# Optimization experiments

Hardware: AMD Instinct MI355X
Metric: run time of the kernel (lower is better)

The kernel has to match this reference:

```python
import jax, jax.numpy as jnp
import numpy as np
import math

HIDDEN = 256
HEADS = 8
HEAD_DIM = HIDDEN // HEADS
SCALE = math.sqrt(HEAD_DIM)


def setup_inputs() -> dict:
    key = jax.random.key(0)
    ks = jax.random.split(key, 10)
    B, N = 2, 4096
    x = jax.random.normal(ks[0], (B, N, HIDDEN), dtype=jnp.float32)
    pos = jax.random.normal(ks[1], (B, N, 3), dtype=jnp.float32)
    s = 1.0 / math.sqrt(HIDDEN)
    Wq = jax.random.normal(ks[2], (HIDDEN, HIDDEN), dtype=jnp.float32) * s
    bq = jnp.zeros((HIDDEN,), dtype=jnp.float32)
    Wk = jax.random.normal(ks[3], (HIDDEN, HIDDEN), dtype=jnp.float32) * s
    bk = jnp.zeros((HIDDEN,), dtype=jnp.float32)
    Wv = jax.random.normal(ks[4], (HIDDEN, HIDDEN), dtype=jnp.float32) * s
    bv = jnp.zeros((HIDDEN,), dtype=jnp.float32)
    Wo = jax.random.normal(ks[5], (HIDDEN, HIDDEN), dtype=jnp.float32) * s
    bo = jnp.zeros((HIDDEN,), dtype=jnp.float32)
    return {"x": x, "pos": pos, "Wq": Wq, "bq": bq, "Wk": Wk, "bk": bk,
            "Wv": Wv, "bv": bv, "Wo": Wo, "bo": bo}


def _pairwise_dist(pos):
    # Euclidean cdist via the norm trick; clip for numerical safety.
    sq = jnp.sum(pos * pos, axis=-1)  # [B, N]
    d2 = sq[:, :, None] + sq[:, None, :] - 2.0 * jnp.einsum('bic,bjc->bij', pos, pos)
    return jnp.sqrt(jnp.maximum(d2, 0.0))  # [B, N, N]


def reference(x, pos, Wq, bq, Wk, bk, Wv, bv, Wo, bo):
    B, N, _ = x.shape
    # projections -> [B, H, N, Dh]
    def split_heads(t):
        return t.reshape(B, N, HEADS, HEAD_DIM).transpose(0, 2, 1, 3)
    q = split_heads(x @ Wq.T + bq)
    k = split_heads(x @ Wk.T + bk)
    v = split_heads(x @ Wv.T + bv)
    scores = jnp.einsum('bhid,bhjd->bhij', q, k) / SCALE
    dist_bias = -_pairwise_dist(pos) / 10.0  # [B, N, N]
    scores = scores + dist_bias[:, None, :, :]
    attn = jax.nn.softmax(scores, axis=-1)
    out = jnp.einsum('bhij,bhjd->bhid', attn, v)
    out = out.transpose(0, 2, 1, 3).reshape(B, N, HIDDEN)
    return out @ Wo.T + bo
```

## Files before the change

### kernel.cpp

```cpp
#include <hip/hip_runtime.h>

#define BATCH 2
#define SEQ   4096
#define HID   256
#define NHEAD 8
#define DH    32
#define THR_L2 11.5f
#define QSCALE 0.25501639769925074f
#define BIASC (-0.14426950408889634f)

typedef __attribute__((ext_vector_type(8))) _Float16 half8;
typedef __attribute__((ext_vector_type(4))) _Float16 half4;
typedef __attribute__((ext_vector_type(2))) __fp16   fp16x2;
typedef __attribute__((ext_vector_type(4))) float    f32x4;
typedef __attribute__((ext_vector_type(4))) unsigned int uint4v;

__device__ __forceinline__ float fast_exp2(float x) {
    return __builtin_amdgcn_exp2f(x);
}

__global__ void cvt_f32_f16(const float* __restrict__ src,
                            _Float16* __restrict__ dst, int n) {
    int i = (blockIdx.x * blockDim.x + threadIdx.x) * 4;
    if (i >= n) return;
    f32x4 v = *reinterpret_cast<const f32x4*>(src + i);
    half4 h;
#pragma unroll
    for (int c = 0; c < 4; ++c) h[c] = (_Float16)v[c];
    *reinterpret_cast<half4*>(dst + i) = h;
}

__global__ void cvt_w4(const float* __restrict__ a, const float* __restrict__ b,
                       const float* __restrict__ c, const float* __restrict__ d,
                       _Float16* __restrict__ dst) {
    const float* srcs[4] = {a, b, c, d};
    const float* s = srcs[blockIdx.y];
    const int i = (blockIdx.x * blockDim.x + threadIdx.x) * 4;
    f32x4 v = *reinterpret_cast<const f32x4*>(s + i);
    half4 h;
#pragma unroll
    for (int k = 0; k < 4; ++k) h[k] = (_Float16)v[k];
    *reinterpret_cast<half4*>(dst + (size_t)blockIdx.y * HID * HID + i) = h;
}

__global__ __launch_bounds__(256) void qkv_proj(
    const _Float16* __restrict__ xh, const _Float16* __restrict__ Wh,
    const float* __restrict__ bq, const float* __restrict__ bk,
    const float* __restrict__ bv,
    _Float16* __restrict__ Qh, _Float16* __restrict__ Kh,
    _Float16* __restrict__ Vt)
{
    const int z   = blockIdx.z;
    const int m0  = blockIdx.x * 64;
    const int n0  = blockIdx.y * 64;
    const int tid = threadIdx.x;
    const int w   = tid >> 6, lane = tid & 63;
    const int lr  = lane & 15, lg = lane >> 4;
    const int wr  = (w >> 1) * 32, wc = (w & 1) * 32;

    const _Float16* Wp = Wh + (size_t)z * HID * HID;
    const float* bias = (z == 0) ? bq : (z == 1) ? bk : bv;

    f32x4 acc[2][2] = {};
    const int ar = m0 + wr + lr;
    const int br = n0 + wc + lr;
#pragma unroll
    for (int ks = 0; ks < 8; ++ks) {
        const int ko = ks * 32 + lg * 8;
        half8 a0 = *reinterpret_cast<const half8*>(xh + (size_t)ar * HID + ko);
        half8 a1 = *reinterpret_cast<const half8*>(xh + (size_t)(ar + 16) * HID + ko);
        half8 b0 = *reinterpret_cast<const half8*>(Wp + (size_t)br * HID + ko);
        half8 b1 = *reinterpret_cast<const half8*>(Wp + (size_t)(br + 16) * HID + ko);
        acc[0][0] = __builtin_amdgcn_mfma_f32_16x16x32_f16(a0, b0, acc[0][0], 0, 0, 0);
        acc[0][1] = __builtin_amdgcn_mfma_f32_16x16x32_f16(a0, b1, acc[0][1], 0, 0, 0);
        acc[1][0] = __builtin_amdgcn_mfma_f32_16x16x32_f16(a1, b0, acc[1][0], 0, 0, 0);
        acc[1][1] = __builtin_amdgcn_mfma_f32_16x16x32_f16(a1, b1, acc[1][1], 0, 0, 0);
    }
#pragma unroll
    for (int mf = 0; mf < 2; ++mf)
#pragma unroll
    for (int nf = 0; nf < 2; ++nf)
#pragma unroll
    for (int r = 0; r < 4; ++r) {
        const int m  = m0 + wr + mf * 16 + lg * 4 + r;
        const int o  = n0 + wc + nf * 16 + lr;
        const int bb = m >> 12, nn = m & (SEQ - 1);
        const int hh = o >> 5,  dd = o & (DH - 1);
        float v = acc[mf][nf][r] + bias[o];
        if (z == 0) {
            Qh[(((size_t)(bb * NHEAD + hh) * SEQ) + nn) * DH + dd] =
                (_Float16)(v * QSCALE);
        } else if (z == 1) {
            Kh[(((size_t)(bb * NHEAD + hh) * SEQ) + nn) * DH + dd] = (_Float16)v;
        } else {
            const int pp = (nn & ~31) | ((nn & 12) << 1) | ((nn & 16) >> 2) | (nn & 3);
            Vt[(((size_t)(bb * NHEAD + hh) * DH) + dd) * SEQ + pp] = (_Float16)v;
        }
    }
}

__device__ __forceinline__ void attn_tile(
    int s, half8 (&kc)[4], half8 (&kn)[4],
    unsigned long long& ka, unsigned long long& va0, unsigned long long& va1,
    half8 aq, const float* __restrict__ biasRow, float* xw,
    float& mrun, float& lsum, f32x4& acc0, f32x4& acc1, int lane, int lg)
{
    half8 vc0, vc1, vc2, vc3;
    asm volatile(
        "global_load_dwordx4 %0, %[va0], off\n\t"
        "global_load_dwordx4 %1, %[va1], off\n\t"
        "global_load_dwordx4 %2, %[va0], off offset:64\n\t"
        "global_load_dwordx4 %3, %[va1], off offset:64\n\t"
        "global_load_dwordx4 %4, %[ka], off\n\t"
        "global_load_dwordx4 %5, %[ka], off offset:1024\n\t"
        "global_load_dwordx4 %6, %[ka], off offset:2048\n\t"
        "global_load_dwordx4 %7, %[ka], off offset:3072"
        : "=&v"(vc0), "=&v"(vc1), "=&v"(vc2), "=&v"(vc3),
          "=&v"(kn[0]), "=&v"(kn[1]), "=&v"(kn[2]), "=&v"(kn[3])
        : [va0]"v"(va0), [va1]"v"(va1), [ka]"v"(ka));
    va0 += 128; va1 += 128; ka += 4096;

    asm volatile("s_waitcnt vmcnt(8)");
    __builtin_amdgcn_sched_barrier(0);
    f32x4 vv[4];
    __builtin_amdgcn_s_setprio(1);
#pragma unroll
    for (int cf = 0; cf < 4; ++cf) {
        f32x4 cb = *reinterpret_cast<const f32x4*>(
            biasRow + s * 64 + cf * 16 + lg * 4);
        vv[cf] = __builtin_amdgcn_mfma_f32_16x16x32_f16(kc[cf], aq, cb, 0, 0, 0);
    }
    __builtin_amdgcn_s_setprio(0);

    float m0 = fmaxf(fmaxf(vv[0][0], vv[0][1]), vv[0][2]);
    float m1 = fmaxf(fmaxf(vv[0][3], vv[1][0]), vv[1][1]);
    float m2 = fmaxf(fmaxf(vv[1][2], vv[1][3]), vv[2][0]);
    float m3 = fmaxf(fmaxf(vv[2][1], vv[2][2]), vv[2][3]);
    float m4 = fmaxf(fmaxf(vv[3][0], vv[3][1]), vv[3][2]);
    float tmax = fmaxf(fmaxf(fmaxf(m0, m1), fmaxf(m2, m3)),
                       fmaxf(m4, vv[3][3]));

    if (!__all(tmax <= mrun + THR_L2)) {
        float tm = tmax;
        tm = fmaxf(tm, __shfl_xor(tm, 16, 64));
        tm = fmaxf(tm, __shfl_xor(tm, 32, 64));
        const float mnew  = fmaxf(mrun, tm);
        const float alpha = fast_exp2(mrun - mnew);
        if (lane < 16) xw[lane] = alpha;
        f32x4 a4 = *reinterpret_cast<const f32x4*>(&xw[lg * 4]);
        lsum *= alpha;
        mrun = mnew;
        acc0 *= a4;
        acc1 *= a4;
    }

    float e00 = fast_exp2(vv[0][0] - mrun), e01 = fast_exp2(vv[0][1] - mrun);
    float e02 = fast_exp2(vv[0][2] - mrun), e03 = fast_exp2(vv[0][3] - mrun);
    float e10 = fast_exp2(vv[1][0] - mrun), e11 = fast_exp2(vv[1][1] - mrun);
    float e12 = fast_exp2(vv[1][2] - mrun), e13 = fast_exp2(vv[1][3] - mrun);
    float e20 = fast_exp2(vv[2][0] - mrun), e21 = fast_exp2(vv[2][1] - mrun);
    float e22 = fast_exp2(vv[2][2] - mrun), e23 = fast_exp2(vv[2][3] - mrun);
    float e30 = fast_exp2(vv[3][0] - mrun), e31 = fast_exp2(vv[3][1] - mrun);
    float e32 = fast_exp2(vv[3][2] - mrun), e33 = fast_exp2(vv[3][3] - mrun);
    lsum += ((e00 + e01) + (e02 + e03)) + ((e10 + e11) + (e12 + e13)) +
            ((e20 + e21) + (e22 + e23)) + ((e30 + e31) + (e32 + e33));

    uint4v u0, u1;
    u0[0] = __builtin_bit_cast(unsigned int, __builtin_amdgcn_cvt_pkrtz(e00, e01));
    u0[1] = __builtin_bit_cast(unsigned int, __builtin_amdgcn_cvt_pkrtz(e02, e03));
    u0[2] = __builtin_bit_cast(unsigned int, __builtin_amdgcn_cvt_pkrtz(e10, e11));
    u0[3] = __builtin_bit_cast(unsigned int, __builtin_amdgcn_cvt_pkrtz(e12, e13));
    u1[0] = __builtin_bit_cast(unsigned int, __builtin_amdgcn_cvt_pkrtz(e20, e21));
    u1[1] = __builtin_bit_cast(unsigned int, __builtin_amdgcn_cvt_pkrtz(e22, e23));
    u1[2] = __builtin_bit_cast(unsigned int, __builtin_amdgcn_cvt_pkrtz(e30, e31));
    u1[3] = __builtin_bit_cast(unsigned int, __builtin_amdgcn_cvt_pkrtz(e32, e33));
    half8 pa0 = __builtin_bit_cast(half8, u0);
    half8 pa1 = __builtin_bit_cast(half8, u1);

    asm volatile("s_waitcnt vmcnt(4)");
    __builtin_amdgcn_sched_barrier(0);
    __builtin_amdgcn_s_setprio(1);
    acc0 = __builtin_amdgcn_mfma_f32_16x16x32_f16(pa0, vc0, acc0, 0, 0, 0);
    acc1 = __builtin_amdgcn_mfma_f32_16x16x32_f16(pa0, vc1, acc1, 0, 0, 0);
    acc0 = __builtin_amdgcn_mfma_f32_16x16x32_f16(pa1, vc2, acc0, 0, 0, 0);
    acc1 = __builtin_amdgcn_mfma_f32_16x16x32_f16(pa1, vc3, acc1, 0, 0, 0);
    __builtin_amdgcn_s_setprio(0);
}

__global__ __launch_bounds__(512, 4) void attn_kernel(
    const _Float16* __restrict__ Qh, const _Float16* __restrict__ Kh,
    const _Float16* __restrict__ Vt, const float* __restrict__ pos,
    _Float16* __restrict__ AO)
{
    __shared__ __align__(16) float pi4[16][4];
    __shared__ __align__(16) float pj4[512][4];
    __shared__ __align__(16) float biasL[16][516];
    __shared__ __align__(16) float xposeL[NHEAD][16];

    const int g    = blockIdx.x;
    const int x    = g & 7;
    const int b    = x >> 2;
    const int i0   = ((g >> 3) * 4 + (x & 3)) * 16;
    const int tid  = threadIdx.x;
    const int w    = tid >> 6;
    const int lane = tid & 63;
    const int lr   = lane & 15, lg = lane >> 4;

    if (tid < 16) {
        const float* p = pos + (size_t)(b * SEQ + i0 + tid) * 3;
        float xx = p[0], yy = p[1], zz = p[2];
        pi4[tid][0] = xx; pi4[tid][1] = yy; pi4[tid][2] = zz;
        pi4[tid][3] = xx * xx + yy * yy + zz * zz;
    }

    const size_t bhh = (size_t)(b * NHEAD + w);
    const half8 aq = *reinterpret_cast<const half8*>(
        Qh + (bhh * SEQ + i0 + lr) * DH + lg * 8);

    unsigned long long ka  = (unsigned long long)(Kh + bhh * SEQ * DH +
                                                  (size_t)lr * DH + lg * 8);
    unsigned long long va0 = (unsigned long long)(Vt + bhh * DH * SEQ +
                                                  (size_t)lr * SEQ + lg * 8);
    unsigned long long va1 = va0 + (size_t)16 * SEQ * 2;

    f32x4 acc0 = {}, acc1 = {};
    float mrun = -1e30f, lsum = 0.f;

    float* xw = &xposeL[w][0];
    const float* biasRow = &biasL[lr][0];

    half8 kA[4], kB[4];
    asm volatile(
        "global_load_dwordx4 %0, %[ka], off\n\t"
        "global_load_dwordx4 %1, %[ka], off offset:1024\n\t"
        "global_load_dwordx4 %2, %[ka], off offset:2048\n\t"
        "global_load_dwordx4 %3, %[ka], off offset:3072"
        : "=&v"(kA[0]), "=&v"(kA[1]), "=&v"(kA[2]), "=&v"(kA[3])
        : [ka]"v"(ka));
    ka += 4096;

    for (int ch = 0; ch < SEQ / 512; ++ch) {
        __syncthreads();
        {
            const float* p = pos + (size_t)(b * SEQ + ch * 512 + tid) * 3;
            float xx = p[0], yy = p[1], zz = p[2];
            pj4[tid][0] = xx; pj4[tid][1] = yy; pj4[tid][2] = zz;
            pj4[tid][3] = xx * xx + yy * yy + zz * zz;
        }
        __syncthreads();
        {
            const int br  = tid & 15;
            const int c0  = (tid >> 4) * 16;
            const float xi = pi4[br][0], yi = pi4[br][1], zi = pi4[br][2], si = pi4[br][3];
#pragma unroll
            for (int k4 = 0; k4 < 4; ++k4) {
                f32x4 o;
#pragma unroll
                for (int k = 0; k < 4; ++k) {
                    const float* pj = &pj4[c0 + k4 * 4 + k][0];
                    float dot = xi * pj[0] + yi * pj[1] + zi * pj[2];
                    float d2  = si + pj[3] - 2.f * dot;
                    o[k] = BIASC * sqrtf(fmaxf(d2, 0.f));
                }
                *reinterpret_cast<f32x4*>(&biasL[br][c0 + k4 * 4]) = o;
            }
        }
        __syncthreads();

        for (int s = 0; s < 4; ++s) {
            attn_tile(2 * s,     kA, kB, ka, va0, va1, aq, biasRow, xw,
                      mrun, lsum, acc0, acc1, lane, lg);
            attn_tile(2 * s + 1, kB, kA, ka, va0, va1, aq, biasRow, xw,
                      mrun, lsum, acc0, acc1, lane, lg);
        }
    }
    asm volatile("s_waitcnt vmcnt(0)");

    lsum += __shfl_xor(lsum, 16, 64);
    lsum += __shfl_xor(lsum, 32, 64);
    const float inv = 1.f / lsum;
    if (lane < 16) xw[lane] = inv;
    f32x4 i4 = *reinterpret_cast<const f32x4*>(&xw[lg * 4]);
#pragma unroll
    for (int t = 0; t < 4; ++t) {
        const size_t row = (size_t)(b * SEQ + i0 + lg * 4 + t) * HID + w * DH;
        AO[row + lr]      = (_Float16)(acc0[t] * i4[t]);
        AO[row + 16 + lr] = (_Float16)(acc1[t] * i4[t]);
    }
}

__global__ __launch_bounds__(256) void out_proj(
    const _Float16* __restrict__ AO, const _Float16* __restrict__ Woh,
    const float* __restrict__ bo, float* __restrict__ out)
{
    const int m0  = blockIdx.x * 64;
    const int n0  = blockIdx.y * 64;
    const int tid = threadIdx.x;
    const int w   = tid >> 6, lane = tid & 63;
    const int lr  = lane & 15, lg = lane >> 4;
    const int wr  = (w >> 1) * 32, wc = (w & 1) * 32;

    f32x4 acc[2][2] = {};
    const int ar = m0 + wr + lr;
    const int br = n0 + wc + lr;
#pragma unroll
    for (int ks = 0; ks < 8; ++ks) {
        const int ko = ks * 32 + lg * 8;
        half8 a0 = *reinterpret_cast<const half8*>(AO + (size_t)ar * HID + ko);
        half8 a1 = *reinterpret_cast<const half8*>(AO + (size_t)(ar + 16) * HID + ko);
        half8 b0 = *reinterpret_cast<const half8*>(Woh + (size_t)br * HID + ko);
        half8 b1 = *reinterpret_cast<const half8*>(Woh + (size_t)(br + 16) * HID + ko);
        acc[0][0] = __builtin_amdgcn_mfma_f32_16x16x32_f16(a0, b0, acc[0][0], 0, 0, 0);
        acc[0][1] = __builtin_amdgcn_mfma_f32_16x16x32_f16(a0, b1, acc[0][1], 0, 0, 0);
        acc[1][0] = __builtin_amdgcn_mfma_f32_16x16x32_f16(a1, b0, acc[1][0], 0, 0, 0);
        acc[1][1] = __builtin_amdgcn_mfma_f32_16x16x32_f16(a1, b1, acc[1][1], 0, 0, 0);
    }
#pragma unroll
    for (int mf = 0; mf < 2; ++mf)
#pragma unroll
    for (int nf = 0; nf < 2; ++nf)
#pragma unroll
    for (int r = 0; r < 4; ++r) {
        const int m = m0 + wr + mf * 16 + lg * 4 + r;
        const int o = n0 + wc + nf * 16 + lr;
        out[(size_t)m * HID + o] = acc[mf][nf][r] + bo[o];
    }
}

extern "C" void kernel_launch(void* const* d_in, const int* in_sizes, int n_in,
                              void* d_out, int out_size, void* d_ws, size_t ws_size,
                              hipStream_t stream)
{
    const float* x   = (const float*)d_in[0];
    const float* pos = (const float*)d_in[1];
    const float* Wq  = (const float*)d_in[2];
    const float* bq  = (const float*)d_in[3];
    const float* Wk  = (const float*)d_in[4];
    const float* bk  = (const float*)d_in[5];
    const float* Wv  = (const float*)d_in[6];
    const float* bv  = (const float*)d_in[7];
    const float* Wo  = (const float*)d_in[8];
    const float* bo  = (const float*)d_in[9];
    float* out = (float*)d_out;

    char* ws = (char*)d_ws;
    _Float16* Qh = (_Float16*)(ws);
    _Float16* Kh = (_Float16*)(ws + (4  << 20));
    _Float16* Vt = (_Float16*)(ws + (8  << 20));
    _Float16* xh = (_Float16*)(ws + (12 << 20));
    _Float16* AO = xh;
    _Float16* Wh = (_Float16*)(ws + (16 << 20));

    const int NX = BATCH * SEQ * HID;
    const int NW = HID * HID;
    cvt_f32_f16<<<NX / 1024, 256, 0, stream>>>(x, xh, NX);
    cvt_w4<<<dim3(NW / 1024, 4), 256, 0, stream>>>(Wq, Wk, Wv, Wo, Wh);

    qkv_proj<<<dim3(BATCH * SEQ / 64, HID / 64, 3), 256, 0, stream>>>(
        xh, Wh, bq, bk, bv, Qh, Kh, Vt);

    attn_kernel<<<512, 512, 0, stream>>>(Qh, Kh, Vt, pos, AO);

    out_proj<<<dim3(BATCH * SEQ / 64, HID / 64), 256, 0, stream>>>(
        AO, Wh + 3 * NW, bo, out);
}
```

Measured before the change: 236.4 us.

## Split attention key range across two wave groups and merge softmax partials

```diff
diff --git a/kernel.cpp b/kernel.cpp
--- a/kernel.cpp
+++ b/kernel.cpp
@@ -187,15 +187,14 @@
     __builtin_amdgcn_s_setprio(0);
 }
 
-__global__ __launch_bounds__(512, 4) void attn_kernel(
+__global__ __launch_bounds__(1024, 4) void attn_kernel(
     const _Float16* __restrict__ Qh, const _Float16* __restrict__ Kh,
     const _Float16* __restrict__ Vt, const float* __restrict__ pos,
     _Float16* __restrict__ AO)
 {
+    __shared__ __align__(16) float smem[10368];
     __shared__ __align__(16) float pi4[16][4];
-    __shared__ __align__(16) float pj4[512][4];
-    __shared__ __align__(16) float biasL[16][516];
-    __shared__ __align__(16) float xposeL[NHEAD][16];
+    __shared__ __align__(16) float xposeL[16][16];
 
     const int g    = blockIdx.x;
     const int x    = g & 7;
@@ -203,8 +202,14 @@
     const int i0   = ((g >> 3) * 4 + (x & 3)) * 16;
     const int tid  = threadIdx.x;
     const int w    = tid >> 6;
+    const int hh   = w & 7;
+    const int jh   = w >> 3;
     const int lane = tid & 63;
     const int lr   = lane & 15, lg = lane >> 4;
+    const int jbase = jh * (SEQ / 2);
+
+    float* pj4   = smem;
+    float* biasL = smem + 2048;
 
     if (tid < 16) {
         const float* p = pos + (size_t)(b * SEQ + i0 + tid) * 3;
@@ -213,21 +218,21 @@
         pi4[tid][3] = xx * xx + yy * yy + zz * zz;
     }
 
-    const size_t bhh = (size_t)(b * NHEAD + w);
+    const size_t bhh = (size_t)(b * NHEAD + hh);
     const half8 aq = *reinterpret_cast<const half8*>(
         Qh + (bhh * SEQ + i0 + lr) * DH + lg * 8);
 
     unsigned long long ka  = (unsigned long long)(Kh + bhh * SEQ * DH +
-                                                  (size_t)lr * DH + lg * 8);
+                                 (size_t)(jbase + lr) * DH + lg * 8);
     unsigned long long va0 = (unsigned long long)(Vt + bhh * DH * SEQ +
-                                                  (size_t)lr * SEQ + lg * 8);
+                                 (size_t)lr * SEQ + jbase + lg * 8);
     unsigned long long va1 = va0 + (size_t)16 * SEQ * 2;
 
     f32x4 acc0 = {}, acc1 = {};
     float mrun = -1e30f, lsum = 0.f;
 
     float* xw = &xposeL[w][0];
-    const float* biasRow = &biasL[lr][0];
+    const float* biasRow = biasL + jh * 4160 + lr * 260;
 
     half8 kA[4], kB[4];
     asm volatile(
@@ -239,35 +244,38 @@
         : [ka]"v"(ka));
     ka += 4096;
 
-    for (int ch = 0; ch < SEQ / 512; ++ch) {
+    for (int ch = 0; ch < (SEQ / 2) / 256; ++ch) {
+        __syncthreads();
+        if (tid < 512) {
+            const int hf = tid >> 8, jc = tid & 255;
+            const float* p = pos +
+                (size_t)(b * SEQ + hf * (SEQ / 2) + ch * 256 + jc) * 3;
+            float xx = p[0], yy = p[1], zz = p[2];
+            float* q = pj4 + (hf * 256 + jc) * 4;
+            q[0] = xx; q[1] = yy; q[2] = zz; q[3] = xx * xx + yy * yy + zz * zz;
+        }
         __syncthreads();
         {
-            const float* p = pos + (size_t)(b * SEQ + ch * 512 + tid) * 3;
-            float xx = p[0], yy = p[1], zz = p[2];
-            pj4[tid][0] = xx; pj4[tid][1] = yy; pj4[tid][2] = zz;
-            pj4[tid][3] = xx * xx + yy * yy + zz * zz;
-        }
-        __syncthreads();
-        {
-            const int br  = tid & 15;
-            const int c0  = (tid >> 4) * 16;
+            const int br = tid & 15;
+            const int hf = (tid >> 4) & 1;
+            const int c0 = (tid >> 5) * 8;
             const float xi = pi4[br][0], yi = pi4[br][1], zi = pi4[br][2], si = pi4[br][3];
 #pragma unroll
-            for (int k4 = 0; k4 < 4; ++k4) {
+            for (int k4 = 0; k4 < 2; ++k4) {
                 f32x4 o;
 #pragma unroll
                 for (int k = 0; k < 4; ++k) {
-                    const float* pj = &pj4[c0 + k4 * 4 + k][0];
+                    const float* pj = pj4 + (hf * 256 + c0 + k4 * 4 + k) * 4;
                     float dot = xi * pj[0] + yi * pj[1] + zi * pj[2];
                     float d2  = si + pj[3] - 2.f * dot;
                     o[k] = BIASC * sqrtf(fmaxf(d2, 0.f));
                 }
-                *reinterpret_cast<f32x4*>(&biasL[br][c0 + k4 * 4]) = o;
+                *reinterpret_cast<f32x4*>(&biasL[hf * 4160 + br * 260 + c0 + k4 * 4]) = o;
             }
         }
         __syncthreads();
 
-        for (int s = 0; s < 4; ++s) {
+        for (int s = 0; s < 2; ++s) {
             attn_tile(2 * s,     kA, kB, ka, va0, va1, aq, biasRow, xw,
                       mrun, lsum, acc0, acc1, lane, lg);
             attn_tile(2 * s + 1, kB, kA, ka, va0, va1, aq, biasRow, xw,
@@ -278,14 +286,38 @@
 
     lsum += __shfl_xor(lsum, 16, 64);
     lsum += __shfl_xor(lsum, 32, 64);
-    const float inv = 1.f / lsum;
-    if (lane < 16) xw[lane] = inv;
-    f32x4 i4 = *reinterpret_cast<const f32x4*>(&xw[lg * 4]);
+
+    __syncthreads();
+    float* accL = smem;
+    float* mlL  = smem + 8192;
+    float* accW = accL + w * 512;
 #pragma unroll
     for (int t = 0; t < 4; ++t) {
-        const size_t row = (size_t)(b * SEQ + i0 + lg * 4 + t) * HID + w * DH;
-        AO[row + lr]      = (_Float16)(acc0[t] * i4[t]);
-        AO[row + 16 + lr] = (_Float16)(acc1[t] * i4[t]);
+        accW[(lg * 4 + t) * 32 + lr]      = acc0[t];
+        accW[(lg * 4 + t) * 32 + 16 + lr] = acc1[t];
+    }
+    if (lane < 16) {
+        mlL[(w * 16 + lane) * 2 + 0] = mrun;
+        mlL[(w * 16 + lane) * 2 + 1] = lsum;
+    }
+    __syncthreads();
+    if (w < 8) {
+#pragma unroll
+        for (int t = 0; t < 4; ++t) {
+            const int row = lg * 4 + t;
+            const float m0 = mlL[(w * 16 + row) * 2],       l0 = mlL[(w * 16 + row) * 2 + 1];
+            const float m1 = mlL[((w + 8) * 16 + row) * 2], l1 = mlL[((w + 8) * 16 + row) * 2 + 1];
+            const float mm = fmaxf(m0, m1);
+            const float e0 = fast_exp2(m0 - mm), e1 = fast_exp2(m1 - mm);
+            const float inv = 1.f / (l0 * e0 + l1 * e1);
+            const size_t rowoff = (size_t)(b * SEQ + i0 + row) * HID + w * DH;
+            AO[rowoff + lr] = (_Float16)(
+                (accL[w * 512 + row * 32 + lr] * e0 +
+                 accL[(w + 8) * 512 + row * 32 + lr] * e1) * inv);
+            AO[rowoff + 16 + lr] = (_Float16)(
+                (accL[w * 512 + row * 32 + 16 + lr] * e0 +
+                 accL[(w + 8) * 512 + row * 32 + 16 + lr] * e1) * inv);
+        }
     }
 }
 
@@ -359,7 +391,7 @@
     qkv_proj<<<dim3(BATCH * SEQ / 64, HID / 64, 3), 256, 0, stream>>>(
         xh, Wh, bq, bk, bv, Qh, Kh, Vt);
 
-    attn_kernel<<<512, 512, 0, stream>>>(Qh, Kh, Vt, pos, AO);
+    attn_kernel<<<512, 1024, 0, stream>>>(Qh, Kh, Vt, pos, AO);
 
     out_proj<<<dim3(BATCH * SEQ / 64, HID / 64), 256, 0, stream>>>(
         AO, Wh + 3 * NW, bo, out);
```

Result: slower. 253.9 us (+7.4%).

## Prefetch V one tile ahead alongside K and relax launch bounds

Applied to the files above, without the earlier changes.

```diff
diff --git a/kernel.cpp b/kernel.cpp
--- a/kernel.cpp
+++ b/kernel.cpp
@@ -100,12 +100,11 @@
 }
 
 __device__ __forceinline__ void attn_tile(
-    int s, half8 (&kc)[4], half8 (&kn)[4],
+    int s, half8 (&kc)[4], half8 (&kn)[4], half8 (&vc)[4], half8 (&vn)[4],
     unsigned long long& ka, unsigned long long& va0, unsigned long long& va1,
     half8 aq, const float* __restrict__ biasRow, float* xw,
     float& mrun, float& lsum, f32x4& acc0, f32x4& acc1, int lane, int lg)
 {
-    half8 vc0, vc1, vc2, vc3;
     asm volatile(
         "global_load_dwordx4 %0, %[va0], off\n\t"
         "global_load_dwordx4 %1, %[va1], off\n\t"
@@ -115,21 +114,24 @@
         "global_load_dwordx4 %5, %[ka], off offset:1024\n\t"
         "global_load_dwordx4 %6, %[ka], off offset:2048\n\t"
         "global_load_dwordx4 %7, %[ka], off offset:3072"
-        : "=&v"(vc0), "=&v"(vc1), "=&v"(vc2), "=&v"(vc3),
+        : "=&v"(vn[0]), "=&v"(vn[1]), "=&v"(vn[2]), "=&v"(vn[3]),
           "=&v"(kn[0]), "=&v"(kn[1]), "=&v"(kn[2]), "=&v"(kn[3])
         : [va0]"v"(va0), [va1]"v"(va1), [ka]"v"(ka));
     va0 += 128; va1 += 128; ka += 4096;
+
+    f32x4 cb0 = *reinterpret_cast<const f32x4*>(biasRow + s * 64 + 0 * 16 + lg * 4);
+    f32x4 cb1 = *reinterpret_cast<const f32x4*>(biasRow + s * 64 + 1 * 16 + lg * 4);
+    f32x4 cb2 = *reinterpret_cast<const f32x4*>(biasRow + s * 64 + 2 * 16 + lg * 4);
+    f32x4 cb3 = *reinterpret_cast<const f32x4*>(biasRow + s * 64 + 3 * 16 + lg * 4);
 
     asm volatile("s_waitcnt vmcnt(8)");
     __builtin_amdgcn_sched_barrier(0);
     f32x4 vv[4];
     __builtin_amdgcn_s_setprio(1);
-#pragma unroll
-    for (int cf = 0; cf < 4; ++cf) {
-        f32x4 cb = *reinterpret_cast<const f32x4*>(
-            biasRow + s * 64 + cf * 16 + lg * 4);
-        vv[cf] = __builtin_amdgcn_mfma_f32_16x16x32_f16(kc[cf], aq, cb, 0, 0, 0);
-    }
+    vv[0] = __builtin_amdgcn_mfma_f32_16x16x32_f16(kc[0], aq, cb0, 0, 0, 0);
+    vv[1] = __builtin_amdgcn_mfma_f32_16x16x32_f16(kc[1], aq, cb1, 0, 0, 0);
+    vv[2] = __builtin_amdgcn_mfma_f32_16x16x32_f16(kc[2], aq, cb2, 0, 0, 0);
+    vv[3] = __builtin_amdgcn_mfma_f32_16x16x32_f16(kc[3], aq, cb3, 0, 0, 0);
     __builtin_amdgcn_s_setprio(0);
 
     float m0 = fmaxf(fmaxf(vv[0][0], vv[0][1]), vv[0][2]);
@@ -177,17 +179,15 @@
     half8 pa0 = __builtin_bit_cast(half8, u0);
     half8 pa1 = __builtin_bit_cast(half8, u1);
 
-    asm volatile("s_waitcnt vmcnt(4)");
-    __builtin_amdgcn_sched_barrier(0);
     __builtin_amdgcn_s_setprio(1);
-    acc0 = __builtin_amdgcn_mfma_f32_16x16x32_f16(pa0, vc0, acc0, 0, 0, 0);
-    acc1 = __builtin_amdgcn_mfma_f32_16x16x32_f16(pa0, vc1, acc1, 0, 0, 0);
-    acc0 = __builtin_amdgcn_mfma_f32_16x16x32_f16(pa1, vc2, acc0, 0, 0, 0);
-    acc1 = __builtin_amdgcn_mfma_f32_16x16x32_f16(pa1, vc3, acc1, 0, 0, 0);
+    acc0 = __builtin_amdgcn_mfma_f32_16x16x32_f16(pa0, vc[0], acc0, 0, 0, 0);
+    acc1 = __builtin_amdgcn_mfma_f32_16x16x32_f16(pa0, vc[1], acc1, 0, 0, 0);
+    acc0 = __builtin_amdgcn_mfma_f32_16x16x32_f16(pa1, vc[2], acc0, 0, 0, 0);
+    acc1 = __builtin_amdgcn_mfma_f32_16x16x32_f16(pa1, vc[3], acc1, 0, 0, 0);
     __builtin_amdgcn_s_setprio(0);
 }
 
-__global__ __launch_bounds__(512, 4) void attn_kernel(
+__global__ __launch_bounds__(512, 2) void attn_kernel(
     const _Float16* __restrict__ Qh, const _Float16* __restrict__ Kh,
     const _Float16* __restrict__ Vt, const float* __restrict__ pos,
     _Float16* __restrict__ AO)
@@ -229,15 +229,20 @@
     float* xw = &xposeL[w][0];
     const float* biasRow = &biasL[lr][0];
 
-    half8 kA[4], kB[4];
+    half8 kA[4], kB[4], vA[4], vB[4];
     asm volatile(
-        "global_load_dwordx4 %0, %[ka], off\n\t"
-        "global_load_dwordx4 %1, %[ka], off offset:1024\n\t"
-        "global_load_dwordx4 %2, %[ka], off offset:2048\n\t"
-        "global_load_dwordx4 %3, %[ka], off offset:3072"
-        : "=&v"(kA[0]), "=&v"(kA[1]), "=&v"(kA[2]), "=&v"(kA[3])
-        : [ka]"v"(ka));
-    ka += 4096;
+        "global_load_dwordx4 %0, %[va0], off\n\t"
+        "global_load_dwordx4 %1, %[va1], off\n\t"
+        "global_load_dwordx4 %2, %[va0], off offset:64\n\t"
+        "global_load_dwordx4 %3, %[va1], off offset:64\n\t"
+        "global_load_dwordx4 %4, %[ka], off\n\t"
+        "global_load_dwordx4 %5, %[ka], off offset:1024\n\t"
+        "global_load_dwordx4 %6, %[ka], off offset:2048\n\t"
+        "global_load_dwordx4 %7, %[ka], off offset:3072"
+        : "=&v"(vA[0]), "=&v"(vA[1]), "=&v"(vA[2]), "=&v"(vA[3]),
+          "=&v"(kA[0]), "=&v"(kA[1]), "=&v"(kA[2]), "=&v"(kA[3])
+        : [va0]"v"(va0), [va1]"v"(va1), [ka]"v"(ka));
+    va0 += 128; va1 += 128; ka += 4096;
 
     for (int ch = 0; ch < SEQ / 512; ++ch) {
         __syncthreads();
@@ -268,9 +273,9 @@
         __syncthreads();
 
         for (int s = 0; s < 4; ++s) {
-            attn_tile(2 * s,     kA, kB, ka, va0, va1, aq, biasRow, xw,
+            attn_tile(2 * s,     kA, kB, vA, vB, ka, va0, va1, aq, biasRow, xw,
                       mrun, lsum, acc0, acc1, lane, lg);
-            attn_tile(2 * s + 1, kB, kA, ka, va0, va1, aq, biasRow, xw,
+            attn_tile(2 * s + 1, kB, kA, vB, vA, ka, va0, va1, aq, biasRow, xw,
                       mrun, lsum, acc0, acc1, lane, lg);
         }
     }
```

Result: no change. 237.3 us (+0.4%).
